# Kernel optimization log

Hardware: AMD Instinct MI355X
Metric: run time of the kernel (lower is better)

The kernel has to match this reference:

```python
import jax, jax.numpy as jnp
import numpy as np

B, T = 65536, 200
H, S, P = 512, 1000, 5
EPS = 1e-6


def setup_inputs() -> dict:
    key = jax.random.key(0)
    ks = jax.random.split(key, 8)
    init = lambda k, shp, fan: (jax.random.normal(k, shp, jnp.float32) / np.float32(np.sqrt(fan)))
    return {
        "X": jax.random.randint(ks[0], (B,), 0, S, dtype=jnp.int32),
        "y": jax.random.randint(ks[1], (B, T), 0, 2, dtype=jnp.int32),
        "embed": init(ks[2], (S, H), 1.0),
        "W1": init(ks[3], (H, H), H), "b1": jnp.zeros((H,), jnp.float32),
        "W2": init(ks[4], (H, H), H), "b2": jnp.zeros((H,), jnp.float32),
        "Wout": init(ks[5], (H, P), H), "bout": jnp.zeros((P,), jnp.float32),
    }


def reference(X, y, embed, W1, b1, W2, b2, Wout, bout):
    # --- MLP over skill embeddings: params (B, 5) = (l, f, g, s, latent0) ---
    e = embed[X]                                    # (B, H)
    h = jax.nn.relu(e @ W1 + b1)                    # num_layers = 2
    h = jax.nn.relu(h @ W2 + b2)
    params = jnp.clip(jax.nn.sigmoid(h @ Wout + bout), EPS, 1.0 - EPS)  # (B, 5)
    l, g, s = params[:, 0], params[:, 2], params[:, 3]
    latent0 = params[:, 4]                          # (B,)

    y_clean = jnp.where(y == -1, 0, y).astype(jnp.float32)  # (B, T)

    # --- BKT latent-update recurrence over T steps ---
    def step(latent, y_t):
        num1 = latent * (1.0 - s)
        correct = num1 + (1.0 - latent) * g
        k_t1 = num1 / correct
        k_t0 = latent * s / (latent * s + (1.0 - latent) * (1.0 - g))
        k_t = jnp.where(y_t > 0.5, k_t1, k_t0)
        nxt = jnp.clip(k_t + (1.0 - k_t) * l, EPS, 1.0 - EPS)
        return nxt, (correct, latent)

    _, (corrects, latents) = jax.lax.scan(step, latent0, y_clean.T)  # (T, B) each
    return corrects.T, latents.T, params
```

## Files before the change

### kernel.cpp

```cpp
#include <hip/hip_runtime.h>


typedef unsigned int uint;
typedef unsigned char uchar;
typedef unsigned short ushort_t;
typedef __attribute__((ext_vector_type(8))) short short8;
typedef __attribute__((ext_vector_type(4))) float f32x4;
typedef __attribute__((ext_vector_type(2))) uint uint2v;

#define SS 1000
#define HH 512
#define TT 200
#define BB_ 65536
#define PP 5

#define OFF_EMB   0
#define OFF_B1    512000
#define OFF_B2    512512
#define OFF_WOUT  513024
#define OFF_BOUT  515584
#define CONV_TOT  515589

__device__ __forceinline__ float b2f(ushort_t u) {
    return __uint_as_float(((uint)u) << 16);
}
__device__ __forceinline__ ushort_t f2b(float f) {
    uint u = __float_as_uint(f);
    uint r = u + 0x7FFFu + ((u >> 16) & 1u);
    return (ushort_t)(r >> 16);
}
__device__ __forceinline__ int detect_bf16(const uint* __restrict__ embed_raw,
                                           int tid) {
    uint w = embed_raw[tid & 63];
    uint e = (w >> 7) & 0xFFu;
    bool pl = (e >= 117u && e <= 130u);
    return __popcll(__ballot(pl)) >= 32 ? 1 : 0;
}
__device__ __forceinline__ ushort_t ld_bf16(const void* src, int idx, int fb) {
    return fb ? ((const ushort_t*)src)[idx] : f2b(((const float*)src)[idx]);
}

__device__ __forceinline__ float bkt_step(float latent, bool yt,
                                          float oms, float omg, float A1,
                                          float A0, float g, float s,
                                          float oml, float l) {
    float num1    = latent * oms;
    float correct = fmaf(latent, A1, g);
    float lats    = latent * s;
    float num = yt ? num1 : lats;
    float den = yt ? correct : fmaf(latent, A0, omg);
    float kt  = num * __builtin_amdgcn_rcpf(den);
    float nxt = fmaf(kt, oml, l);
    return fminf(fmaxf(nxt, 1e-6f), 1.f - 1e-6f);
}

__global__ __launch_bounds__(256) void prep_kernel(
    const void* __restrict__ embed, const void* __restrict__ W1,
    const void* __restrict__ b1,    const void* __restrict__ W2,
    const void* __restrict__ b2,    const void* __restrict__ Wout,
    const void* __restrict__ bout,
    ushort_t* __restrict__ conv, ushort_t* __restrict__ WT1,
    ushort_t* __restrict__ WT2)
{
    int tid = threadIdx.x;
    int fb = detect_bf16((const uint*)embed, tid);
    int bx = blockIdx.x;
    if (bx < 504) {
        int i = (bx * 256 + tid) * 4;
        if (i < CONV_TOT) {
            const void* src; int off;
            if      (i < OFF_B1)   { src = embed; off = i; }
            else if (i < OFF_B2)   { src = b1;    off = i - OFF_B1; }
            else if (i < OFF_WOUT) { src = b2;    off = i - OFF_B2; }
            else if (i < OFF_BOUT) { src = Wout;  off = i - OFF_WOUT; }
            else                   { src = bout;  off = i - OFF_BOUT; }
            if (i + 3 < CONV_TOT) {
                ushort_t o0, o1, o2, o3;
                if (fb) {
                    ushort4 v = *(const ushort4*)((const ushort_t*)src + off);
                    o0 = v.x; o1 = v.y; o2 = v.z; o3 = v.w;
                } else {
                    float4 v = *(const float4*)((const float*)src + off);
                    o0 = f2b(v.x); o1 = f2b(v.y); o2 = f2b(v.z); o3 = f2b(v.w);
                }
                ushort4 o; o.x = o0; o.y = o1; o.z = o2; o.w = o3;
                *(ushort4*)(conv + i) = o;
            } else {
                for (int k = 0; i + k < CONV_TOT; k++)
                    conv[i + k] = ld_bf16(src, off + k, fb);
            }
        }
    } else {
        __shared__ ushort_t t[32][33];
        int bi = bx - 504;
        const void* W = bi < 256 ? W1 : W2;
        ushort_t* WT = bi < 256 ? WT1 : WT2;
        int ti = bi & 255;
        int k0 = (ti & 15) * 32, n0 = (ti >> 4) * 32;
        int tx = tid & 31, ty = tid >> 5;
        #pragma unroll
        for (int i = ty; i < 32; i += 8)
            t[i][tx] = ld_bf16(W, (k0 + i) * HH + n0 + tx, fb);
        __syncthreads();
        #pragma unroll
        for (int i = ty; i < 32; i += 8)
            WT[(n0 + i) * HH + k0 + tx] = t[tx][i];
    }
}

__global__ __launch_bounds__(256) void mlp_layer(
    const ushort_t* __restrict__ A, const ushort_t* __restrict__ WT,
    const ushort_t* __restrict__ bias, ushort_t* __restrict__ H, int Mclamp)
{
    int tid = threadIdx.x;
    int lane = tid & 63;
    int wave = tid >> 6;
    int m_base = blockIdx.x * 64 + wave * 16;
    int n_base = blockIdx.y * 16;
    int lrow = lane & 15;
    int q = lane >> 4;
    int rowA = m_base + lrow; if (rowA > Mclamp) rowA = Mclamp;

    const short8* Ap = (const short8*)(A + (size_t)rowA * HH) + q;
    const short8* Bp = (const short8*)(WT + (size_t)(n_base + lrow) * HH) + q;

    f32x4 acc = {0.f, 0.f, 0.f, 0.f};
    #pragma unroll 8
    for (int kk = 0; kk < 16; kk++) {
        short8 a = Ap[kk * 4];
        short8 b = Bp[kk * 4];
        acc = __builtin_amdgcn_mfma_f32_16x16x32_bf16(a, b, acc, 0, 0, 0);
    }

    int orow = m_base + q * 4;
    int n = n_base + lrow;
    float bb = b2f(bias[n]);
    #pragma unroll
    for (int r = 0; r < 4; r++) {
        float v = acc[r] + bb;
        H[(size_t)(orow + r) * HH + n] = f2b(fmaxf(v, 0.f));
    }
}

__global__ __launch_bounds__(256) void params_kernel(
    const ushort_t* __restrict__ h2, const ushort_t* __restrict__ conv,
    float* __restrict__ table)
{
    int wid = blockIdx.x * 4 + (threadIdx.x >> 6);
    int lane = threadIdx.x & 63;
    if (wid >= SS * PP) return;
    int row = wid / PP, p = wid - row * PP;
    const ushort_t* Wout = conv + OFF_WOUT;
    const ushort_t* bout = conv + OFF_BOUT;
    const short8* hr = (const short8*)(h2 + (size_t)row * HH);
    short8 h = hr[lane];
    float acc = 0.f;
    #pragma unroll
    for (int j = 0; j < 8; j++) {
        int k = lane * 8 + j;
        acc += b2f((ushort_t)h[j]) * b2f(Wout[k * PP + p]);
    }
    #pragma unroll
    for (int m = 32; m; m >>= 1) acc += __shfl_xor(acc, m);
    if (lane == 0) {
        float x = acc + b2f(bout[p]);
        float sg = 1.f / (1.f + expf(-x));
        sg = fminf(fmaxf(sg, 1e-6f), 1.f - 1e-6f);
        table[(size_t)row * 8 + p] = sg;
    }
}

__global__ __launch_bounds__(256) void scan_kernel(
    const int* __restrict__ X, const int* __restrict__ y,
    const float* __restrict__ table, const uint* __restrict__ embed_raw,
    void* __restrict__ out)
{
    __shared__ __align__(16) float stg[32 * 200];
    __shared__ uchar ybit[32 * 50];
    __shared__ float pA1[32], pG[32];
    int tid = threadIdx.x;
    int rbase = blockIdx.x * 32;
    int fb = detect_bf16(embed_raw, tid);

    for (int idx = tid; idx < 1600; idx += 256) {
        int r = idx / 50, k = idx - r * 50;
        int4 v = *(const int4*)(y + (size_t)(rbase + r) * TT + k * 4);
        ybit[r * 50 + k] = (uchar)((uint)(v.x == 1) | ((uint)(v.y == 1) << 1) |
                                   ((uint)(v.z == 1) << 2) | ((uint)(v.w == 1) << 3));
    }
    __syncthreads();

    int lane = tid & 63, wv = tid >> 6;
    if (lane < 8) {
        int r = wv * 8 + lane;
        int rg = rbase + r;
        int xi = X[rg]; xi = xi < 0 ? 0 : (xi >= SS ? SS - 1 : xi);
        float l      = table[xi * 8 + 0];
        float p1     = table[xi * 8 + 1];
        float g      = table[xi * 8 + 2];
        float s      = table[xi * 8 + 3];
        float L0     = table[xi * 8 + 4];
        float oms = 1.f - s, omg = 1.f - g, oml = 1.f - l;
        float A1 = 1.f - s - g, A0 = s + g - 1.f;
        pA1[r] = A1; pG[r] = g;

        if (fb) {
            ushort_t* pp = (ushort_t*)out + 2ull * BB_ * TT + (size_t)rg * 5;
            pp[0] = f2b(l); pp[1] = f2b(p1); pp[2] = f2b(g);
            pp[3] = f2b(s); pp[4] = f2b(L0);
        } else {
            float* pp = (float*)out + 2ull * BB_ * TT + (size_t)rg * 5;
            pp[0] = l; pp[1] = p1; pp[2] = g; pp[3] = s; pp[4] = L0;
        }

        float latent = L0;
        const uchar* yb = &ybit[r * 50];
        float* srow = &stg[r * 200];
        for (int k = 0; k < 50; k++) {
            uint nib = yb[k];
            #pragma unroll
            for (int i = 0; i < 4; i++) {
                srow[k * 4 + i] = latent;
                latent = bkt_step(latent, (nib >> i) & 1u,
                                  oms, omg, A1, A0, g, s, oml, l);
            }
        }
    }
    __syncthreads();

    const f32x4* src = (const f32x4*)stg;
    if (!fb) {
        f32x4* dc = (f32x4*)((float*)out + (size_t)rbase * TT);
        f32x4* dl = (f32x4*)((float*)out + (size_t)BB_ * TT + (size_t)rbase * TT);
        for (int idx = tid; idx < 1600; idx += 256) {
            int r = idx / 50;
            f32x4 v = src[idx];
            float A1 = pA1[r], g = pG[r];
            f32x4 c;
            c[0] = fmaf(v[0], A1, g); c[1] = fmaf(v[1], A1, g);
            c[2] = fmaf(v[2], A1, g); c[3] = fmaf(v[3], A1, g);
            __builtin_nontemporal_store(v, dl + idx);
            __builtin_nontemporal_store(c, dc + idx);
        }
    } else {
        uint2v* dc = (uint2v*)((ushort_t*)out + (size_t)rbase * TT);
        uint2v* dl = (uint2v*)((ushort_t*)out + (size_t)BB_ * TT + (size_t)rbase * TT);
        for (int idx = tid; idx < 1600; idx += 256) {
            int r = idx / 50;
            f32x4 v = src[idx];
            float A1 = pA1[r], g = pG[r];
            uint2v lv, cv;
            lv[0] = (uint)f2b(v[0]) | ((uint)f2b(v[1]) << 16);
            lv[1] = (uint)f2b(v[2]) | ((uint)f2b(v[3]) << 16);
            cv[0] = (uint)f2b(fmaf(v[0], A1, g)) | ((uint)f2b(fmaf(v[1], A1, g)) << 16);
            cv[1] = (uint)f2b(fmaf(v[2], A1, g)) | ((uint)f2b(fmaf(v[3], A1, g)) << 16);
            __builtin_nontemporal_store(lv, dl + idx);
            __builtin_nontemporal_store(cv, dc + idx);
        }
    }
}

extern "C" void kernel_launch(void* const* d_in, const int* in_sizes, int n_in,
                              void* d_out, int out_size, void* d_ws, size_t ws_size,
                              hipStream_t stream) {
    const int* X = (const int*)d_in[0];
    const int* y = (const int*)d_in[1];

    char* ws = (char*)d_ws;
    ushort_t* conv  = (ushort_t*)(ws);
    ushort_t* WT1   = (ushort_t*)(ws + 1048576);
    ushort_t* WT2   = (ushort_t*)(ws + 1572864);
    ushort_t* h1    = (ushort_t*)(ws + 2097152);
    ushort_t* h2    = (ushort_t*)(ws + 3145728);
    float*    table = (float*)(ws + 4194304);

    prep_kernel<<<dim3(1016, 1, 1), 256, 0, stream>>>(
        d_in[2], d_in[3], d_in[4], d_in[5], d_in[6], d_in[7], d_in[8],
        conv, WT1, WT2);
    mlp_layer<<<dim3(16, 32, 1), 256, 0, stream>>>(conv + OFF_EMB, WT1, conv + OFF_B1, h1, SS - 1);
    mlp_layer<<<dim3(16, 32, 1), 256, 0, stream>>>(h1, WT2, conv + OFF_B2, h2, 1023);
    params_kernel<<<dim3(1250, 1, 1), 256, 0, stream>>>(h2, conv, table);
    scan_kernel<<<dim3(2048, 1, 1), 256, 0, stream>>>(
        X, y, table, (const uint*)d_in[2], (void*)d_out);
}
```

Baseline: 212.2 us.

## Fuse output projection into second MLP layer via atomic partial dot products

Drops the separate params kernel by folding the Wout projection into the second GEMM's epilogue. Each tile reduces its partial dot products across lanes with shuffles and atomically adds them into a zeroed raw logit table. The bias, sigmoid and clamp are deferred to the scan kernel. This removes one launch and the h2 round trip, at the cost of 20 atomics per output row per column tile and nondeterministic summation order.

```diff
diff --git a/kernel.cpp b/kernel.cpp
--- a/kernel.cpp
+++ b/kernel.cpp
@@ -17,9 +17,7 @@
 #define OFF_EMB   0
 #define OFF_B1    512000
 #define OFF_B2    512512
-#define OFF_WOUT  513024
-#define OFF_BOUT  515584
-#define CONV_TOT  515589
+#define CONV_TOT  513024
 
 __device__ __forceinline__ float b2f(ushort_t u) {
     return __uint_as_float(((uint)u) << 16);
@@ -38,6 +36,9 @@
 }
 __device__ __forceinline__ ushort_t ld_bf16(const void* src, int idx, int fb) {
     return fb ? ((const ushort_t*)src)[idx] : f2b(((const float*)src)[idx]);
+}
+__device__ __forceinline__ float ldf(const void* src, int idx, int fb) {
+    return fb ? b2f(((const ushort_t*)src)[idx]) : ((const float*)src)[idx];
 }
 
 __device__ __forceinline__ float bkt_step(float latent, bool yt,
@@ -57,42 +58,33 @@
 __global__ __launch_bounds__(256) void prep_kernel(
     const void* __restrict__ embed, const void* __restrict__ W1,
     const void* __restrict__ b1,    const void* __restrict__ W2,
-    const void* __restrict__ b2,    const void* __restrict__ Wout,
-    const void* __restrict__ bout,
+    const void* __restrict__ b2,
     ushort_t* __restrict__ conv, ushort_t* __restrict__ WT1,
-    ushort_t* __restrict__ WT2)
+    ushort_t* __restrict__ WT2,  float* __restrict__ tableRaw)
 {
     int tid = threadIdx.x;
     int fb = detect_bf16((const uint*)embed, tid);
     int bx = blockIdx.x;
-    if (bx < 504) {
+    if (bx < 501) {
         int i = (bx * 256 + tid) * 4;
         if (i < CONV_TOT) {
             const void* src; int off;
             if      (i < OFF_B1)   { src = embed; off = i; }
             else if (i < OFF_B2)   { src = b1;    off = i - OFF_B1; }
-            else if (i < OFF_WOUT) { src = b2;    off = i - OFF_B2; }
-            else if (i < OFF_BOUT) { src = Wout;  off = i - OFF_WOUT; }
-            else                   { src = bout;  off = i - OFF_BOUT; }
-            if (i + 3 < CONV_TOT) {
-                ushort_t o0, o1, o2, o3;
-                if (fb) {
-                    ushort4 v = *(const ushort4*)((const ushort_t*)src + off);
-                    o0 = v.x; o1 = v.y; o2 = v.z; o3 = v.w;
-                } else {
-                    float4 v = *(const float4*)((const float*)src + off);
-                    o0 = f2b(v.x); o1 = f2b(v.y); o2 = f2b(v.z); o3 = f2b(v.w);
-                }
-                ushort4 o; o.x = o0; o.y = o1; o.z = o2; o.w = o3;
-                *(ushort4*)(conv + i) = o;
+            else                   { src = b2;    off = i - OFF_B2; }
+            ushort4 o;
+            if (fb) {
+                ushort4 v = *(const ushort4*)((const ushort_t*)src + off);
+                o = v;
             } else {
-                for (int k = 0; i + k < CONV_TOT; k++)
-                    conv[i + k] = ld_bf16(src, off + k, fb);
+                float4 v = *(const float4*)((const float*)src + off);
+                o.x = f2b(v.x); o.y = f2b(v.y); o.z = f2b(v.z); o.w = f2b(v.w);
             }
-        }
-    } else {
+            *(ushort4*)(conv + i) = o;
+        }
+    } else if (bx < 1013) {
         __shared__ ushort_t t[32][33];
-        int bi = bx - 504;
+        int bi = bx - 501;
         const void* W = bi < 256 ? W1 : W2;
         ushort_t* WT = bi < 256 ? WT1 : WT2;
         int ti = bi & 255;
@@ -105,6 +97,9 @@
         #pragma unroll
         for (int i = ty; i < 32; i += 8)
             WT[(n0 + i) * HH + k0 + tx] = t[tx][i];
+    } else {
+        int idx = (bx - 1013) * 256 + tid;
+        if (idx < SS * PP) tableRaw[idx] = 0.f;
     }
 }
 
@@ -142,38 +137,78 @@
     }
 }
 
-__global__ __launch_bounds__(256) void params_kernel(
-    const ushort_t* __restrict__ h2, const ushort_t* __restrict__ conv,
-    float* __restrict__ table)
+__global__ __launch_bounds__(256) void mlp2_kernel(
+    const ushort_t* __restrict__ A, const ushort_t* __restrict__ WT,
+    const ushort_t* __restrict__ bias, const void* __restrict__ Wout,
+    const uint* __restrict__ embed_raw, float* __restrict__ tableRaw)
 {
-    int wid = blockIdx.x * 4 + (threadIdx.x >> 6);
-    int lane = threadIdx.x & 63;
-    if (wid >= SS * PP) return;
-    int row = wid / PP, p = wid - row * PP;
-    const ushort_t* Wout = conv + OFF_WOUT;
-    const ushort_t* bout = conv + OFF_BOUT;
-    const short8* hr = (const short8*)(h2 + (size_t)row * HH);
-    short8 h = hr[lane];
-    float acc = 0.f;
+    int tid = threadIdx.x;
+    int fb = detect_bf16(embed_raw, tid);
+    int lane = tid & 63;
+    int wave = tid >> 6;
+    int m_base = blockIdx.x * 64 + wave * 16;
+    int n_base = blockIdx.y * 16;
+    int lrow = lane & 15;
+    int q = lane >> 4;
+    int rowA = m_base + lrow; if (rowA > 1023) rowA = 1023;
+
+    const short8* Ap = (const short8*)(A + (size_t)rowA * HH) + q;
+    const short8* Bp = (const short8*)(WT + (size_t)(n_base + lrow) * HH) + q;
+
+    f32x4 acc = {0.f, 0.f, 0.f, 0.f};
+    #pragma unroll 8
+    for (int kk = 0; kk < 16; kk++) {
+        short8 a = Ap[kk * 4];
+        short8 b = Bp[kk * 4];
+        acc = __builtin_amdgcn_mfma_f32_16x16x32_bf16(a, b, acc, 0, 0, 0);
+    }
+
+    int orow = m_base + q * 4;
+    int n = n_base + lrow;
+    float bb = b2f(bias[n]);
+    float h[4];
     #pragma unroll
-    for (int j = 0; j < 8; j++) {
-        int k = lane * 8 + j;
-        acc += b2f((ushort_t)h[j]) * b2f(Wout[k * PP + p]);
-    }
+    for (int r = 0; r < 4; r++)
+        h[r] = fmaxf(acc[r] + bb, 0.f);
+
+    float w[5];
+    if (fb) {
+        const ushort_t* W16 = (const ushort_t*)Wout;
+        #pragma unroll
+        for (int p = 0; p < 5; p++) w[p] = b2f(W16[n * 5 + p]);
+    } else {
+        const float* W32 = (const float*)Wout;
+        #pragma unroll
+        for (int p = 0; p < 5; p++) w[p] = W32[n * 5 + p];
+    }
+
+    float sdot[5][4];
     #pragma unroll
-    for (int m = 32; m; m >>= 1) acc += __shfl_xor(acc, m);
-    if (lane == 0) {
-        float x = acc + b2f(bout[p]);
-        float sg = 1.f / (1.f + expf(-x));
-        sg = fminf(fmaxf(sg, 1e-6f), 1.f - 1e-6f);
-        table[(size_t)row * 8 + p] = sg;
+    for (int p = 0; p < 5; p++)
+        #pragma unroll
+        for (int r = 0; r < 4; r++)
+            sdot[p][r] = h[r] * w[p];
+    #pragma unroll
+    for (int m = 1; m < 16; m <<= 1)
+        #pragma unroll
+        for (int p = 0; p < 5; p++)
+            #pragma unroll
+            for (int r = 0; r < 4; r++)
+                sdot[p][r] += __shfl_xor(sdot[p][r], m);
+
+    if (lrow == 0 && orow < SS) {
+        #pragma unroll
+        for (int r = 0; r < 4; r++)
+            #pragma unroll
+            for (int p = 0; p < 5; p++)
+                atomicAdd(&tableRaw[(orow + r) * 5 + p], sdot[p][r]);
     }
 }
 
 __global__ __launch_bounds__(256) void scan_kernel(
     const int* __restrict__ X, const int* __restrict__ y,
-    const float* __restrict__ table, const uint* __restrict__ embed_raw,
-    void* __restrict__ out)
+    const float* __restrict__ tableRaw, const void* __restrict__ bout,
+    const uint* __restrict__ embed_raw, void* __restrict__ out)
 {
     __shared__ __align__(16) float stg[32 * 200];
     __shared__ uchar ybit[32 * 50];
@@ -195,22 +230,26 @@
         int r = wv * 8 + lane;
         int rg = rbase + r;
         int xi = X[rg]; xi = xi < 0 ? 0 : (xi >= SS ? SS - 1 : xi);
-        float l      = table[xi * 8 + 0];
-        float p1     = table[xi * 8 + 1];
-        float g      = table[xi * 8 + 2];
-        float s      = table[xi * 8 + 3];
-        float L0     = table[xi * 8 + 4];
+        float lg[5];
+        #pragma unroll
+        for (int p = 0; p < 5; p++) {
+            float logit = tableRaw[xi * 5 + p] + ldf(bout, p, fb);
+            float sg = 1.f / (1.f + expf(-logit));
+            lg[p] = fminf(fmaxf(sg, 1e-6f), 1.f - 1e-6f);
+        }
+        float l = lg[0], g = lg[2], s = lg[3], L0 = lg[4];
         float oms = 1.f - s, omg = 1.f - g, oml = 1.f - l;
         float A1 = 1.f - s - g, A0 = s + g - 1.f;
         pA1[r] = A1; pG[r] = g;
 
         if (fb) {
             ushort_t* pp = (ushort_t*)out + 2ull * BB_ * TT + (size_t)rg * 5;
-            pp[0] = f2b(l); pp[1] = f2b(p1); pp[2] = f2b(g);
-            pp[3] = f2b(s); pp[4] = f2b(L0);
+            #pragma unroll
+            for (int p = 0; p < 5; p++) pp[p] = f2b(lg[p]);
         } else {
             float* pp = (float*)out + 2ull * BB_ * TT + (size_t)rg * 5;
-            pp[0] = l; pp[1] = p1; pp[2] = g; pp[3] = s; pp[4] = L0;
+            #pragma unroll
+            for (int p = 0; p < 5; p++) pp[p] = lg[p];
         }
 
         float latent = L0;
@@ -267,19 +306,19 @@
     const int* y = (const int*)d_in[1];
 
     char* ws = (char*)d_ws;
-    ushort_t* conv  = (ushort_t*)(ws);
-    ushort_t* WT1   = (ushort_t*)(ws + 1048576);
-    ushort_t* WT2   = (ushort_t*)(ws + 1572864);
-    ushort_t* h1    = (ushort_t*)(ws + 2097152);
-    ushort_t* h2    = (ushort_t*)(ws + 3145728);
-    float*    table = (float*)(ws + 4194304);
-
-    prep_kernel<<<dim3(1016, 1, 1), 256, 0, stream>>>(
-        d_in[2], d_in[3], d_in[4], d_in[5], d_in[6], d_in[7], d_in[8],
-        conv, WT1, WT2);
-    mlp_layer<<<dim3(16, 32, 1), 256, 0, stream>>>(conv + OFF_EMB, WT1, conv + OFF_B1, h1, SS - 1);
-    mlp_layer<<<dim3(16, 32, 1), 256, 0, stream>>>(h1, WT2, conv + OFF_B2, h2, 1023);
-    params_kernel<<<dim3(1250, 1, 1), 256, 0, stream>>>(h2, conv, table);
+    ushort_t* conv     = (ushort_t*)(ws);
+    ushort_t* WT1      = (ushort_t*)(ws + 1048576);
+    ushort_t* WT2      = (ushort_t*)(ws + 1572864);
+    ushort_t* h1       = (ushort_t*)(ws + 2097152);
+    float*    tableRaw = (float*)(ws + 3145728);
+
+    prep_kernel<<<dim3(1033, 1, 1), 256, 0, stream>>>(
+        d_in[2], d_in[3], d_in[4], d_in[5], d_in[6],
+        conv, WT1, WT2, tableRaw);
+    mlp_layer<<<dim3(16, 32, 1), 256, 0, stream>>>(
+        conv + OFF_EMB, WT1, conv + OFF_B1, h1, SS - 1);
+    mlp2_kernel<<<dim3(16, 32, 1), 256, 0, stream>>>(
+        h1, WT2, conv + OFF_B2, d_in[7], (const uint*)d_in[2], tableRaw);
     scan_kernel<<<dim3(2048, 1, 1), 256, 0, stream>>>(
-        X, y, table, (const uint*)d_in[2], (void*)d_out);
-}
+        X, y, tableRaw, d_in[8], (const uint*)d_in[2], (void*)d_out);
+}
```

Measured after the change: 225.4 us. +6.2%, slower.

## Split BKT scan into checkpoint pass and parallel 8-segment replay pass

Applied to the files above, without the earlier changes.

Splits the scan into two kernels. The first packs y bits and runs the full 200-step recurrence once per row, saving the latent at eight checkpoints along with 25-bit masks. The second replays each 25-step segment from its checkpoint, using all 256 threads instead of 8 per wave, then writes the outputs with ordinary stores instead of nontemporal stores. This trades more parallelism in the output-writing kernel for a second serial pass, an extra launch and extra workspace traffic.

```diff
diff --git a/kernel.cpp b/kernel.cpp
--- a/kernel.cpp
+++ b/kernel.cpp
@@ -75,15 +75,13 @@
             else if (i < OFF_BOUT) { src = Wout;  off = i - OFF_WOUT; }
             else                   { src = bout;  off = i - OFF_BOUT; }
             if (i + 3 < CONV_TOT) {
-                ushort_t o0, o1, o2, o3;
+                ushort4 o;
                 if (fb) {
-                    ushort4 v = *(const ushort4*)((const ushort_t*)src + off);
-                    o0 = v.x; o1 = v.y; o2 = v.z; o3 = v.w;
+                    o = *(const ushort4*)((const ushort_t*)src + off);
                 } else {
                     float4 v = *(const float4*)((const float*)src + off);
-                    o0 = f2b(v.x); o1 = f2b(v.y); o2 = f2b(v.z); o3 = f2b(v.w);
+                    o.x = f2b(v.x); o.y = f2b(v.y); o.z = f2b(v.z); o.w = f2b(v.w);
                 }
-                ushort4 o; o.x = o0; o.y = o1; o.z = o2; o.w = o3;
                 *(ushort4*)(conv + i) = o;
             } else {
                 for (int k = 0; i + k < CONV_TOT; k++)
@@ -170,61 +168,100 @@
     }
 }
 
-__global__ __launch_bounds__(256) void scan_kernel(
+__global__ __launch_bounds__(256) void scan_a(
     const int* __restrict__ X, const int* __restrict__ y,
-    const float* __restrict__ table, const uint* __restrict__ embed_raw,
-    void* __restrict__ out)
+    const float* __restrict__ table,
+    float* __restrict__ cpA, uint* __restrict__ maskA)
+{
+    __shared__ uchar ybit[128 * 50];
+    int tid = threadIdx.x;
+    int rbase = blockIdx.x * 128;
+
+    for (int idx = tid; idx < 6400; idx += 256) {
+        int r = idx / 50, k = idx - r * 50;
+        int4 v = *(const int4*)(y + (size_t)(rbase + r) * TT + k * 4);
+        ybit[r * 50 + k] = (uchar)((uint)(v.x == 1) | ((uint)(v.y == 1) << 1) |
+                                   ((uint)(v.z == 1) << 2) | ((uint)(v.w == 1) << 3));
+    }
+    __syncthreads();
+
+    if (tid < 128) {
+        int rg = rbase + tid;
+        int xi = X[rg]; xi = xi < 0 ? 0 : (xi >= SS ? SS - 1 : xi);
+        float l      = table[xi * 8 + 0];
+        float g      = table[xi * 8 + 2];
+        float s      = table[xi * 8 + 3];
+        float latent = table[xi * 8 + 4];
+        float oms = 1.f - s, omg = 1.f - g, oml = 1.f - l;
+        float A1 = 1.f - s - g, A0 = s + g - 1.f;
+        const uchar* yb = &ybit[tid * 50];
+        float cp[8]; uint mk[8];
+        #pragma unroll
+        for (int w = 0; w < 8; w++) {
+            cp[w] = latent;
+            uint m = 0;
+            #pragma unroll
+            for (int k = 0; k < 7; k++) {
+                if (k * 4 >= 25) break;
+                uint nib = yb[w * 25 / 4 + 0];
+            }
+            #pragma unroll
+            for (int i = 0; i < 25; i++) {
+                int t_ = w * 25 + i;
+                uint bit = (ybit[tid * 50 + (t_ >> 2)] >> (t_ & 3)) & 1u;
+                m |= bit << i;
+                latent = bkt_step(latent, bit, oms, omg, A1, A0, g, s, oml, l);
+            }
+            mk[w] = m;
+        }
+        #pragma unroll
+        for (int w = 0; w < 8; w++) {
+            cpA[(size_t)w * BB_ + rg]   = cp[w];
+            maskA[(size_t)w * BB_ + rg] = mk[w];
+        }
+    }
+}
+
+__global__ __launch_bounds__(256) void scan_b(
+    const int* __restrict__ X, const float* __restrict__ table,
+    const float* __restrict__ cpA, const uint* __restrict__ maskA,
+    const uint* __restrict__ embed_raw, void* __restrict__ out)
 {
     __shared__ __align__(16) float stg[32 * 200];
-    __shared__ uchar ybit[32 * 50];
     __shared__ float pA1[32], pG[32];
     int tid = threadIdx.x;
     int rbase = blockIdx.x * 32;
     int fb = detect_bf16(embed_raw, tid);
 
-    for (int idx = tid; idx < 1600; idx += 256) {
-        int r = idx / 50, k = idx - r * 50;
-        int4 v = *(const int4*)(y + (size_t)(rbase + r) * TT + k * 4);
-        ybit[r * 50 + k] = (uchar)((uint)(v.x == 1) | ((uint)(v.y == 1) << 1) |
-                                   ((uint)(v.z == 1) << 2) | ((uint)(v.w == 1) << 3));
-    }
-    __syncthreads();
-
-    int lane = tid & 63, wv = tid >> 6;
-    if (lane < 8) {
-        int r = wv * 8 + lane;
-        int rg = rbase + r;
-        int xi = X[rg]; xi = xi < 0 ? 0 : (xi >= SS ? SS - 1 : xi);
-        float l      = table[xi * 8 + 0];
-        float p1     = table[xi * 8 + 1];
-        float g      = table[xi * 8 + 2];
-        float s      = table[xi * 8 + 3];
-        float L0     = table[xi * 8 + 4];
-        float oms = 1.f - s, omg = 1.f - g, oml = 1.f - l;
-        float A1 = 1.f - s - g, A0 = s + g - 1.f;
-        pA1[r] = A1; pG[r] = g;
-
-        if (fb) {
-            ushort_t* pp = (ushort_t*)out + 2ull * BB_ * TT + (size_t)rg * 5;
-            pp[0] = f2b(l); pp[1] = f2b(p1); pp[2] = f2b(g);
-            pp[3] = f2b(s); pp[4] = f2b(L0);
-        } else {
-            float* pp = (float*)out + 2ull * BB_ * TT + (size_t)rg * 5;
-            pp[0] = l; pp[1] = p1; pp[2] = g; pp[3] = s; pp[4] = L0;
-        }
-
-        float latent = L0;
-        const uchar* yb = &ybit[r * 50];
-        float* srow = &stg[r * 200];
-        for (int k = 0; k < 50; k++) {
-            uint nib = yb[k];
-            #pragma unroll
-            for (int i = 0; i < 4; i++) {
-                srow[k * 4 + i] = latent;
-                latent = bkt_step(latent, (nib >> i) & 1u,
-                                  oms, omg, A1, A0, g, s, oml, l);
-            }
-        }
+    int r = tid >> 3, j = tid & 7;
+    int rg = rbase + r;
+    int xi = X[rg]; xi = xi < 0 ? 0 : (xi >= SS ? SS - 1 : xi);
+    float l  = table[xi * 8 + 0];
+    float p1 = table[xi * 8 + 1];
+    float g  = table[xi * 8 + 2];
+    float s  = table[xi * 8 + 3];
+    float L0 = table[xi * 8 + 4];
+
+    if (j == 0) { pA1[r] = 1.f - s - g; pG[r] = g; }
+
+    if (j < 5) {
+        float pv = j == 0 ? l : j == 1 ? p1 : j == 2 ? g : j == 3 ? s : L0;
+        size_t po = 2ull * BB_ * TT + (size_t)rg * 5 + j;
+        if (fb) ((ushort_t*)out)[po] = f2b(pv);
+        else    ((float*)out)[po] = pv;
+    }
+
+    float latent = cpA[(size_t)j * BB_ + rg];
+    uint  u      = maskA[(size_t)j * BB_ + rg];
+    float oms = 1.f - s, omg = 1.f - g, oml = 1.f - l;
+    float A1 = 1.f - s - g, A0 = s + g - 1.f;
+
+    int sbase = r * 200 + j * 25;
+    #pragma unroll
+    for (int i = 0; i < 25; i++) {
+        stg[sbase + i] = latent;
+        latent = bkt_step(latent, (u >> i) & 1u,
+                          oms, omg, A1, A0, g, s, oml, l);
     }
     __syncthreads();
 
@@ -233,29 +270,29 @@
         f32x4* dc = (f32x4*)((float*)out + (size_t)rbase * TT);
         f32x4* dl = (f32x4*)((float*)out + (size_t)BB_ * TT + (size_t)rbase * TT);
         for (int idx = tid; idx < 1600; idx += 256) {
-            int r = idx / 50;
+            int rr = idx / 50;
             f32x4 v = src[idx];
-            float A1 = pA1[r], g = pG[r];
+            float a1 = pA1[rr], gg = pG[rr];
             f32x4 c;
-            c[0] = fmaf(v[0], A1, g); c[1] = fmaf(v[1], A1, g);
-            c[2] = fmaf(v[2], A1, g); c[3] = fmaf(v[3], A1, g);
-            __builtin_nontemporal_store(v, dl + idx);
-            __builtin_nontemporal_store(c, dc + idx);
+            c[0] = fmaf(v[0], a1, gg); c[1] = fmaf(v[1], a1, gg);
+            c[2] = fmaf(v[2], a1, gg); c[3] = fmaf(v[3], a1, gg);
+            dl[idx] = v;
+            dc[idx] = c;
         }
     } else {
         uint2v* dc = (uint2v*)((ushort_t*)out + (size_t)rbase * TT);
         uint2v* dl = (uint2v*)((ushort_t*)out + (size_t)BB_ * TT + (size_t)rbase * TT);
         for (int idx = tid; idx < 1600; idx += 256) {
-            int r = idx / 50;
+            int rr = idx / 50;
             f32x4 v = src[idx];
-            float A1 = pA1[r], g = pG[r];
+            float a1 = pA1[rr], gg = pG[rr];
             uint2v lv, cv;
             lv[0] = (uint)f2b(v[0]) | ((uint)f2b(v[1]) << 16);
             lv[1] = (uint)f2b(v[2]) | ((uint)f2b(v[3]) << 16);
-            cv[0] = (uint)f2b(fmaf(v[0], A1, g)) | ((uint)f2b(fmaf(v[1], A1, g)) << 16);
-            cv[1] = (uint)f2b(fmaf(v[2], A1, g)) | ((uint)f2b(fmaf(v[3], A1, g)) << 16);
-            __builtin_nontemporal_store(lv, dl + idx);
-            __builtin_nontemporal_store(cv, dc + idx);
+            cv[0] = (uint)f2b(fmaf(v[0], a1, gg)) | ((uint)f2b(fmaf(v[1], a1, gg)) << 16);
+            cv[1] = (uint)f2b(fmaf(v[2], a1, gg)) | ((uint)f2b(fmaf(v[3], a1, gg)) << 16);
+            dl[idx] = lv;
+            dc[idx] = cv;
         }
     }
 }
@@ -273,13 +310,18 @@
     ushort_t* h1    = (ushort_t*)(ws + 2097152);
     ushort_t* h2    = (ushort_t*)(ws + 3145728);
     float*    table = (float*)(ws + 4194304);
+    float*    cpA   = (float*)(ws + 4227072);
+    uint*     maskA = (uint*)(ws + 6324224);
 
     prep_kernel<<<dim3(1016, 1, 1), 256, 0, stream>>>(
         d_in[2], d_in[3], d_in[4], d_in[5], d_in[6], d_in[7], d_in[8],
         conv, WT1, WT2);
-    mlp_layer<<<dim3(16, 32, 1), 256, 0, stream>>>(conv + OFF_EMB, WT1, conv + OFF_B1, h1, SS - 1);
-    mlp_layer<<<dim3(16, 32, 1), 256, 0, stream>>>(h1, WT2, conv + OFF_B2, h2, 1023);
+    mlp_layer<<<dim3(16, 32, 1), 256, 0, stream>>>(
+        conv + OFF_EMB, WT1, conv + OFF_B1, h1, SS - 1);
+    mlp_layer<<<dim3(16, 32, 1), 256, 0, stream>>>(
+        h1, WT2, conv + OFF_B2, h2, 1023);
     params_kernel<<<dim3(1250, 1, 1), 256, 0, stream>>>(h2, conv, table);
-    scan_kernel<<<dim3(2048, 1, 1), 256, 0, stream>>>(
-        X, y, table, (const uint*)d_in[2], (void*)d_out);
-}
+    scan_a<<<dim3(512, 1, 1), 256, 0, stream>>>(X, y, table, cpA, maskA);
+    scan_b<<<dim3(2048, 1, 1), 256, 0, stream>>>(
+        X, table, cpA, maskA, (const uint*)d_in[2], (void*)d_out);
+}
```

After: 203.4 us. 1.04x faster.
